# Kernel tuning notes

Hardware: AMD Instinct MI355X
Metric: run time of the kernel (lower is better)

Reference implementation:

```python
import jax, jax.numpy as jnp
import numpy as np

B, S, D, MEM, STRIDE = 8, 8192, 128, 128, 64

def setup_inputs() -> dict:
    key = jax.random.key(0)
    ks = jax.random.split(key, 6)
    scale = 0.01  # matches nn.init.normal_(w, 0.0, 0.01)
    x = jax.random.normal(ks[0], (B, S, D), dtype=jnp.float32)
    Wq = scale * jax.random.normal(ks[1], (D, D), dtype=jnp.float32)
    Wk = scale * jax.random.normal(ks[2], (D, D), dtype=jnp.float32)
    Wv = scale * jax.random.normal(ks[3], (MEM, D), dtype=jnp.float32)
    Wg_w = jnp.zeros((1, D), dtype=jnp.float32)       # W_g weight init zeros
    Wg_b = jnp.full((1,), -2.0, dtype=jnp.float32)    # W_g bias init -2.0
    Wout = scale * jax.random.normal(ks[4], (D, MEM), dtype=jnp.float32)
    return {"x": x, "Wq": Wq, "Wk": Wk, "Wv": Wv, "Wg_w": Wg_w, "Wg_b": Wg_b, "Wout": Wout}

def reference(x, Wq, Wk, Wv, Wg_w, Wg_b, Wout):
    b, s, d = x.shape
    nC = s // STRIDE  # S assumed divisible by stride
    q = x @ Wq.T                                  # [B,S,D]
    k = x @ Wk.T                                  # [B,S,D]
    v = x @ Wv.T                                  # [B,S,MEM]
    g = jax.nn.sigmoid(x @ Wg_w.T + Wg_b)         # [B,S,1]
    # chunk: leading scan axis nC
    qc = q.reshape(b, nC, STRIDE, d).transpose(1, 0, 2, 3)
    kc = k.reshape(b, nC, STRIDE, d).transpose(1, 0, 2, 3)
    vc = v.reshape(b, nC, STRIDE, MEM).transpose(1, 0, 2, 3)
    gc = g.reshape(b, nC, STRIDE, 1).transpose(1, 0, 2, 3)

    def step(M, chunk):
        qch, kch, vch, gch = chunk
        reads = jnp.einsum('bsd,bdm->bsm', qch, M)              # read before write
        write = jnp.einsum('bsd,bsm->bdm', kch * gch, vch)      # gated outer-product
        avg_gate = gch.mean(axis=1, keepdims=True)              # [B,1,1]
        M_new = (1.0 - avg_gate) * M + write
        return M_new, reads

    M0 = jnp.zeros((b, d, MEM), dtype=x.dtype)
    _, reads = jax.lax.scan(step, M0, (qc, kc, vc, gc))         # [nC,B,STRIDE,MEM]
    out = reads.transpose(1, 0, 2, 3).reshape(b, s, MEM)
    return out @ Wout.T                                         # [B,S,D]
```

## Files before the change

kernel.cpp:

```cpp
#include <hip/hip_runtime.h>

#define Bn 8
#define Sn 8192
#define Dn 128
#define NCn 128

typedef _Float16 f16;
typedef f16 f16x2 __attribute__((ext_vector_type(2)));
typedef f16 f16x4 __attribute__((ext_vector_type(4)));
typedef float f32x4 __attribute__((ext_vector_type(4)));

static __device__ __forceinline__ f32x4 mfma16(f16x4 a, f16x4 b, f32x4 c) {
  return __builtin_amdgcn_mfma_f32_16x16x16f16(a, b, c, 0, 0, 0);
}

union UU { uint4 u; f16x2 h[4]; f16x4 q[2]; };


__global__ __launch_bounds__(64) void k_prep(
    const float* __restrict__ Wq, const float* __restrict__ Wk,
    const float* __restrict__ Wv, const float* __restrict__ Wout,
    f16* __restrict__ Amat, f16* __restrict__ r2) {
  const int blk = blockIdx.x;
  const int which = blk >> 6;
  const int t = blk & 63, ti = t >> 3, tj = t & 7;
  const int lane = threadIdx.x & 63, r16 = lane & 15, g4 = lane >> 4;
  f32x4 acc = {};
  if (which == 0) {
#pragma unroll
    for (int kk = 0; kk < 8; ++kk) {
      f16x4 af, bf;
#pragma unroll
      for (int j = 0; j < 4; ++j) {
        af[j] = (f16)Wq[(kk * 16 + g4 * 4 + j) * 128 + ti * 16 + r16];
        bf[j] = (f16)Wk[(kk * 16 + g4 * 4 + j) * 128 + tj * 16 + r16];
      }
      acc = mfma16(af, bf, acc);
    }
  } else {
#pragma unroll
    for (int kk = 0; kk < 8; ++kk) {
      f16x4 af, bf;
      float4 a4 = *(const float4*)(Wout + (ti * 16 + r16) * 128 + kk * 16 + g4 * 4);
      af[0] = (f16)a4.x; af[1] = (f16)a4.y; af[2] = (f16)a4.z; af[3] = (f16)a4.w;
#pragma unroll
      for (int j = 0; j < 4; ++j)
        bf[j] = (f16)Wv[(kk * 16 + g4 * 4 + j) * 128 + tj * 16 + r16];
      acc = mfma16(af, bf, acc);
    }
  }
  f16* dst = which ? r2 : Amat;
#pragma unroll
  for (int j = 0; j < 4; ++j)
    dst[(ti * 16 + g4 * 4 + j) * 128 + tj * 16 + r16] = (f16)acc[j];
}

__global__ __launch_bounds__(512, 8) void k_phase1(
    const float* __restrict__ x, const float* __restrict__ gw, const float* __restrict__ gb,
    const f16* __restrict__ Amat, const f16* __restrict__ r2,
    f16x4* __restrict__ wtg, float* __restrict__ gavg, f16* __restrict__ xh) {
  __shared__ __align__(16) f16 Xs[64][136];
  __shared__ __align__(16) f16x4 vP[2048];
  __shared__ float gs[64];
  const int h = blockIdx.x;
  const int grp = h & 127, m = h >> 7;
  const int b = grp >> 4, seg = grp & 15;
  const int c = seg * 8 + m;
  const int tid = threadIdx.x;
  {
    int s = tid >> 3, sub = tid & 7;
    const float* xrow = x + ((size_t)b * Sn + (size_t)c * 64 + s) * Dn;
    f16* xhrow = xh + (size_t)(b * NCn + c) * 8192 + s * 128;
    float gpart = 0.f;
#pragma unroll
    for (int i = 0; i < 4; ++i) {
      int col = sub * 4 + i * 32;
      float4 v = *(const float4*)(xrow + col);
      float4 g = *(const float4*)(gw + col);
      gpart += v.x * g.x + v.y * g.y + v.z * g.z + v.w * g.w;
      f16x4 hh = {(f16)v.x, (f16)v.y, (f16)v.z, (f16)v.w};
      *(f16x4*)&Xs[s][col] = hh;
      *(f16x4*)&xhrow[col] = hh;
    }
    gpart += __shfl_xor(gpart, 1);
    gpart += __shfl_xor(gpart, 2);
    gpart += __shfl_xor(gpart, 4);
    if (sub == 0) gs[s] = 1.f / (1.f + __expf(-(gpart + gb[0])));
  }
  __syncthreads();
  if (tid == 0) {
    float sum = 0.f;
#pragma unroll
    for (int i = 0; i < 64; ++i) sum += gs[i];
    gavg[b * NCn + c] = sum * (1.f / 64.f);
  }
  const int w = tid >> 6, lane = tid & 63, r16 = lane & 15, g4 = lane >> 4;
  f32x4 uacc[4] = {}, vacc[4] = {};
#pragma unroll
  for (int kk = 0; kk < 8; ++kk) {
    f16x4 bu = *(const f16x4*)&Amat[(w * 16 + r16) * 128 + kk * 16 + g4 * 4];
    f16x4 bv = *(const f16x4*)&r2[(w * 16 + r16) * 128 + kk * 16 + g4 * 4];
#pragma unroll
    for (int mr = 0; mr < 4; ++mr) {
      f16x4 af = *(f16x4*)&Xs[mr * 16 + r16][kk * 16 + g4 * 4];
      uacc[mr] = mfma16(af, bu, uacc[mr]);
      vacc[mr] = mfma16(af, bv, vacc[mr]);
    }
  }
  f16x4 ua[4];
#pragma unroll
  for (int mr = 0; mr < 4; ++mr) {
    float g0 = gs[mr * 16 + g4 * 4 + 0], g1 = gs[mr * 16 + g4 * 4 + 1];
    float g2 = gs[mr * 16 + g4 * 4 + 2], g3 = gs[mr * 16 + g4 * 4 + 3];
    f16x4 uh = {(f16)(uacc[mr][0] * g0), (f16)(uacc[mr][1] * g1),
                (f16)(uacc[mr][2] * g2), (f16)(uacc[mr][3] * g3)};
    ua[mr] = uh;
    f16x4 vh = {(f16)vacc[mr][0], (f16)vacc[mr][1], (f16)vacc[mr][2], (f16)vacc[mr][3]};
    vP[(mr * 8 + w) * 64 + lane] = vh;
  }
  __syncthreads();
  f32x4 z[8] = {};
#pragma unroll
  for (int ks = 0; ks < 4; ++ks)
#pragma unroll
    for (int ct = 0; ct < 8; ++ct)
      z[ct] = mfma16(ua[ks], vP[(ks * 8 + ct) * 64 + lane], z[ct]);
  f16x4* wdst = wtg + (size_t)(b * NCn + c) * 4096;
#pragma unroll
  for (int ct = 0; ct < 8; ++ct) {
    f16x4 zh = {(f16)z[ct][0], (f16)z[ct][1], (f16)z[ct][2], (f16)z[ct][3]};
    wdst[(w * 8 + ct) * 64 + lane] = zh;
  }
}

__global__ __launch_bounds__(256) void k_scan(
    const uint* __restrict__ wtg, const float* __restrict__ gavg, uint* __restrict__ pbuf) {
  const int blk = blockIdx.x;
  const int b = blk >> 5;
  const int e = (blk & 31) * 256 + threadIdx.x;
  const uint* wp = wtg + (size_t)b * (NCn * 8192) + e;
  uint* pp = pbuf + (size_t)b * (15 * 8192) + e;
  const float* ga = gavg + b * NCn;
  float M0 = 0.f, M1 = 0.f;
  uint ubuf[32];
  float abuf[32];
#pragma unroll
  for (int i = 0; i < 32; ++i) {
    ubuf[i] = wp[(size_t)i * 8192];
    abuf[i] = ga[i];
  }
  for (int g = 0; g < 4; ++g) {
    uint un[32];
    float an[32];
    if (g < 3) {
#pragma unroll
      for (int i = 0; i < 32; ++i) {
        un[i] = wp[(size_t)((g + 1) * 32 + i) * 8192];
        an[i] = ga[(g + 1) * 32 + i];
      }
    }
#pragma unroll
    for (int i = 0; i < 32; ++i) {
      int cc = g * 32 + i;
      f16x2 wv = __builtin_bit_cast(f16x2, ubuf[i]);
      float dd = 1.f - abuf[i];
      M0 = dd * M0 + (float)wv[0];
      M1 = dd * M1 + (float)wv[1];
      if ((cc & 7) == 7 && cc < 120) {
        f16x2 mv = {(f16)M0, (f16)M1};
        pp[(size_t)(cc >> 3) * 8192] = __builtin_bit_cast(uint, mv);
      }
    }
    if (g < 3) {
#pragma unroll
      for (int i = 0; i < 32; ++i) { ubuf[i] = un[i]; abuf[i] = an[i]; }
    }
  }
}

__global__ __launch_bounds__(512, 4) void k_outseg(
    const f16* __restrict__ xh, const uint4* __restrict__ wtg4,
    const uint4* __restrict__ pbuf4, const float* __restrict__ gavg,
    float* __restrict__ outp) {
  __shared__ __align__(16) f16 Xs[64][136];
  __shared__ __align__(16) float Mf[4096];
  __shared__ __align__(16) f16x4 Mh4[1024];
  const int blk = blockIdx.x;
  const int q = blk & 3, seg = (blk >> 2) & 15, b = blk >> 6;
  const int tid = threadIdx.x;
  const int w = tid >> 6, lane = tid & 63, r16 = lane & 15, g4 = lane >> 4;
  const int mr = w & 3, tq = w >> 2;

  const int lt = tid >> 5;
  const int gtile = (lt >> 1) * 8 + q * 2 + (lt & 1);
  const int slot = tid & 31;

  float dseg[8];
#pragma unroll
  for (int t = 0; t < 8; ++t) dseg[t] = 1.f - gavg[b * NCn + seg * 8 + t];

  float4* Mf4 = (float4*)Mf;
  if (seg > 0) {
    UU z; z.u = pbuf4[(size_t)(b * 15 + seg - 1) * 2048 + gtile * 32 + slot];
#pragma unroll
    for (int h2 = 0; h2 < 2; ++h2) {
      float4 mv = {(float)z.h[2 * h2][0], (float)z.h[2 * h2][1],
                   (float)z.h[2 * h2 + 1][0], (float)z.h[2 * h2 + 1][1]};
      Mf4[tid * 2 + h2] = mv;
    }
  } else {
    float4 zz = {0.f, 0.f, 0.f, 0.f};
    Mf4[tid * 2] = zz;
    Mf4[tid * 2 + 1] = zz;
  }

  const uint4* Zseg = wtg4 + (size_t)(b * NCn + seg * 8) * 2048;
  const f16* xhseg = xh + (size_t)(b * NCn + seg * 8) * 8192;

  for (int m = 0; m < 8; ++m) {
    {
      const uint4* xs4 = (const uint4*)(xhseg + (size_t)m * 8192);
      int row = tid >> 3, col = (tid & 7) * 16;
      uint4 a = xs4[tid * 2];
      uint4 bq = xs4[tid * 2 + 1];
      *(uint4*)&Xs[row][col] = a;
      *(uint4*)&Xs[row][col + 8] = bq;
    }
#pragma unroll
    for (int h2 = 0; h2 < 2; ++h2) {
      float4 mv = Mf4[tid * 2 + h2];
      f16x4 hh = {(f16)mv.x, (f16)mv.y, (f16)mv.z, (f16)mv.w};
      Mh4[tid * 2 + h2] = hh;
    }
    __syncthreads();

    f32x4 acc = {};
#pragma unroll
    for (int kk = 0; kk < 8; ++kk) {
      f16x4 af = *(f16x4*)&Xs[mr * 16 + r16][kk * 16 + g4 * 4];
      f16x4 bf = Mh4[(kk * 2 + tq) * 64 + lane];
      acc = mfma16(af, bf, acc);
    }

    {
      UU z; z.u = Zseg[(size_t)m * 2048 + gtile * 32 + slot];
      float dd = dseg[m];
#pragma unroll
      for (int h2 = 0; h2 < 2; ++h2) {
        float4 mv = Mf4[tid * 2 + h2];
        mv.x = dd * mv.x + (float)z.h[2 * h2][0];
        mv.y = dd * mv.y + (float)z.h[2 * h2][1];
        mv.z = dd * mv.z + (float)z.h[2 * h2 + 1][0];
        mv.w = dd * mv.w + (float)z.h[2 * h2 + 1][1];
        Mf4[tid * 2 + h2] = mv;
      }
    }

    {
      const int c = seg * 8 + m;
      float* ob = outp + ((size_t)b * Sn + (size_t)c * 64 + mr * 16 + g4 * 4) * Dn +
                  (q * 2 + tq) * 16 + r16;
#pragma unroll
      for (int j = 0; j < 4; ++j) ob[(size_t)j * Dn] = acc[j];
    }
    __syncthreads();
  }
}

extern "C" void kernel_launch(void* const* d_in, const int* in_sizes, int n_in,
                              void* d_out, int out_size, void* d_ws, size_t ws_size,
                              hipStream_t stream) {
  const float* x = (const float*)d_in[0];
  const float* Wq = (const float*)d_in[1];
  const float* Wk = (const float*)d_in[2];
  const float* Wv = (const float*)d_in[3];
  const float* gw = (const float*)d_in[4];
  const float* gb = (const float*)d_in[5];
  const float* Wout = (const float*)d_in[6];

  char* ws = (char*)d_ws;
  f16* Amat = (f16*)(ws + 0);
  f16* r2 = (f16*)(ws + 32768);
  float* gavg = (float*)(ws + 65536);
  f16* wtg = (f16*)(ws + 69632);
  f16* pbuf = (f16*)(ws + 33624064);
  f16* xh = (f16*)(ws + 37556224);

  k_prep<<<dim3(128), dim3(64), 0, stream>>>(Wq, Wk, Wv, Wout, Amat, r2);
  k_phase1<<<dim3(Bn * NCn), dim3(512), 0, stream>>>(x, gw, gb, Amat, r2, (f16x4*)wtg,
                                                     gavg, xh);
  k_scan<<<dim3(256), dim3(256), 0, stream>>>((const uint*)wtg, gavg, (uint*)pbuf);
  k_outseg<<<dim3(512), dim3(512), 0, stream>>>(xh, (const uint4*)wtg, (const uint4*)pbuf,
                                                gavg, (float*)d_out);
}
```

Baseline: 64.92 us.

## Fold chunk-state scan into output kernel and prefetch next x tile

Removes the separate scan kernel and its checkpoint buffer. Each output block now recomputes its starting memory state by folding all preceding chunk writes from the weighted-outer-product buffer. Blocks are ordered so that the longest-prefix segments launch first. The next chunk's x tile and the current Z tile are also prefetched into registers ahead of the MFMA loop. This saves a launch and a global round trip, but adds redundant prefix reads that grow with the segment index (up to 120 chunk loads per thread for the last segment).

```diff
diff --git a/kernel.cpp b/kernel.cpp
--- a/kernel.cpp
+++ b/kernel.cpp
@@ -133,60 +133,16 @@
   }
 }
 
-__global__ __launch_bounds__(256) void k_scan(
-    const uint* __restrict__ wtg, const float* __restrict__ gavg, uint* __restrict__ pbuf) {
-  const int blk = blockIdx.x;
-  const int b = blk >> 5;
-  const int e = (blk & 31) * 256 + threadIdx.x;
-  const uint* wp = wtg + (size_t)b * (NCn * 8192) + e;
-  uint* pp = pbuf + (size_t)b * (15 * 8192) + e;
-  const float* ga = gavg + b * NCn;
-  float M0 = 0.f, M1 = 0.f;
-  uint ubuf[32];
-  float abuf[32];
-#pragma unroll
-  for (int i = 0; i < 32; ++i) {
-    ubuf[i] = wp[(size_t)i * 8192];
-    abuf[i] = ga[i];
-  }
-  for (int g = 0; g < 4; ++g) {
-    uint un[32];
-    float an[32];
-    if (g < 3) {
-#pragma unroll
-      for (int i = 0; i < 32; ++i) {
-        un[i] = wp[(size_t)((g + 1) * 32 + i) * 8192];
-        an[i] = ga[(g + 1) * 32 + i];
-      }
-    }
-#pragma unroll
-    for (int i = 0; i < 32; ++i) {
-      int cc = g * 32 + i;
-      f16x2 wv = __builtin_bit_cast(f16x2, ubuf[i]);
-      float dd = 1.f - abuf[i];
-      M0 = dd * M0 + (float)wv[0];
-      M1 = dd * M1 + (float)wv[1];
-      if ((cc & 7) == 7 && cc < 120) {
-        f16x2 mv = {(f16)M0, (f16)M1};
-        pp[(size_t)(cc >> 3) * 8192] = __builtin_bit_cast(uint, mv);
-      }
-    }
-    if (g < 3) {
-#pragma unroll
-      for (int i = 0; i < 32; ++i) { ubuf[i] = un[i]; abuf[i] = an[i]; }
-    }
-  }
-}
-
-__global__ __launch_bounds__(512, 4) void k_outseg(
+__global__ __launch_bounds__(512, 4) void k_outfold(
     const f16* __restrict__ xh, const uint4* __restrict__ wtg4,
-    const uint4* __restrict__ pbuf4, const float* __restrict__ gavg,
-    float* __restrict__ outp) {
+    const float* __restrict__ gavg, float* __restrict__ outp) {
   __shared__ __align__(16) f16 Xs[64][136];
   __shared__ __align__(16) float Mf[4096];
   __shared__ __align__(16) f16x4 Mh4[1024];
   const int blk = blockIdx.x;
-  const int q = blk & 3, seg = (blk >> 2) & 15, b = blk >> 6;
+  const int seg = 15 - (blk >> 5);
+  const int sub5 = blk & 31;
+  const int b = sub5 >> 2, q = sub5 & 3;
   const int tid = threadIdx.x;
   const int w = tid >> 6, lane = tid & 63, r16 = lane & 15, g4 = lane >> 4;
   const int mr = w & 3, tq = w >> 2;
@@ -195,37 +151,43 @@
   const int gtile = (lt >> 1) * 8 + q * 2 + (lt & 1);
   const int slot = tid & 31;
 
+  float4 P0 = {0.f, 0.f, 0.f, 0.f}, P1 = {0.f, 0.f, 0.f, 0.f};
+  {
+    const uint4* Zb = wtg4 + (size_t)(b * NCn) * 2048 + gtile * 32 + slot;
+    const float* ga = gavg + b * NCn;
+    const int nt = seg * 8;
+#pragma unroll 4
+    for (int t = 0; t < nt; ++t) {
+      UU z; z.u = Zb[(size_t)t * 2048];
+      float dd = 1.f - ga[t];
+      P0.x = dd * P0.x + (float)z.h[0][0];
+      P0.y = dd * P0.y + (float)z.h[0][1];
+      P0.z = dd * P0.z + (float)z.h[1][0];
+      P0.w = dd * P0.w + (float)z.h[1][1];
+      P1.x = dd * P1.x + (float)z.h[2][0];
+      P1.y = dd * P1.y + (float)z.h[2][1];
+      P1.z = dd * P1.z + (float)z.h[3][0];
+      P1.w = dd * P1.w + (float)z.h[3][1];
+    }
+  }
+  float4* Mf4 = (float4*)Mf;
+  Mf4[tid * 2] = P0;
+  Mf4[tid * 2 + 1] = P1;
+
   float dseg[8];
 #pragma unroll
   for (int t = 0; t < 8; ++t) dseg[t] = 1.f - gavg[b * NCn + seg * 8 + t];
-
-  float4* Mf4 = (float4*)Mf;
-  if (seg > 0) {
-    UU z; z.u = pbuf4[(size_t)(b * 15 + seg - 1) * 2048 + gtile * 32 + slot];
-#pragma unroll
-    for (int h2 = 0; h2 < 2; ++h2) {
-      float4 mv = {(float)z.h[2 * h2][0], (float)z.h[2 * h2][1],
-                   (float)z.h[2 * h2 + 1][0], (float)z.h[2 * h2 + 1][1]};
-      Mf4[tid * 2 + h2] = mv;
-    }
-  } else {
-    float4 zz = {0.f, 0.f, 0.f, 0.f};
-    Mf4[tid * 2] = zz;
-    Mf4[tid * 2 + 1] = zz;
-  }
 
   const uint4* Zseg = wtg4 + (size_t)(b * NCn + seg * 8) * 2048;
   const f16* xhseg = xh + (size_t)(b * NCn + seg * 8) * 8192;
+  const int xrow = tid >> 3, xcol = (tid & 7) * 16;
+
+  uint4 xa = ((const uint4*)xhseg)[tid * 2];
+  uint4 xb2 = ((const uint4*)xhseg)[tid * 2 + 1];
 
   for (int m = 0; m < 8; ++m) {
-    {
-      const uint4* xs4 = (const uint4*)(xhseg + (size_t)m * 8192);
-      int row = tid >> 3, col = (tid & 7) * 16;
-      uint4 a = xs4[tid * 2];
-      uint4 bq = xs4[tid * 2 + 1];
-      *(uint4*)&Xs[row][col] = a;
-      *(uint4*)&Xs[row][col + 8] = bq;
-    }
+    *(uint4*)&Xs[xrow][xcol] = xa;
+    *(uint4*)&Xs[xrow][xcol + 8] = xb2;
 #pragma unroll
     for (int h2 = 0; h2 < 2; ++h2) {
       float4 mv = Mf4[tid * 2 + h2];
@@ -234,6 +196,14 @@
     }
     __syncthreads();
 
+    UU z;
+    z.u = Zseg[(size_t)m * 2048 + gtile * 32 + slot];
+    if (m < 7) {
+      const uint4* xn = (const uint4*)(xhseg + (size_t)(m + 1) * 8192);
+      xa = xn[tid * 2];
+      xb2 = xn[tid * 2 + 1];
+    }
+
     f32x4 acc = {};
 #pragma unroll
     for (int kk = 0; kk < 8; ++kk) {
@@ -243,7 +213,6 @@
     }
 
     {
-      UU z; z.u = Zseg[(size_t)m * 2048 + gtile * 32 + slot];
       float dd = dseg[m];
 #pragma unroll
       for (int h2 = 0; h2 < 2; ++h2) {
@@ -283,13 +252,11 @@
   f16* r2 = (f16*)(ws + 32768);
   float* gavg = (float*)(ws + 65536);
   f16* wtg = (f16*)(ws + 69632);
-  f16* pbuf = (f16*)(ws + 33624064);
   f16* xh = (f16*)(ws + 37556224);
 
   k_prep<<<dim3(128), dim3(64), 0, stream>>>(Wq, Wk, Wv, Wout, Amat, r2);
   k_phase1<<<dim3(Bn * NCn), dim3(512), 0, stream>>>(x, gw, gb, Amat, r2, (f16x4*)wtg,
                                                      gavg, xh);
-  k_scan<<<dim3(256), dim3(256), 0, stream>>>((const uint*)wtg, gavg, (uint*)pbuf);
-  k_outseg<<<dim3(512), dim3(512), 0, stream>>>(xh, (const uint4*)wtg, (const uint4*)pbuf,
-                                                gavg, (float*)d_out);
-}
+  k_outfold<<<dim3(512), dim3(512), 0, stream>>>(xh, (const uint4*)wtg, gavg,
+                                                 (float*)d_out);
+}
```

New measurement: 62.56 us. 3.6% less time.
